# Kernel optimization log

Hardware: AMD Instinct MI355X
Metric: run time of the kernel (lower is better)

## Reference

```python
import jax, jax.numpy as jnp
import numpy as np

EPS = 1e-5


def setup_inputs() -> dict:
    key = jax.random.key(0)
    k_x, k_y, k_w, k_b = jax.random.split(key, 4)
    B, IN, OUT = 16384, 1024, 1024
    x = jax.random.normal(k_x, (B, IN), dtype=jnp.float32)
    y = jax.random.normal(k_y, (B, OUT), dtype=jnp.float32)
    # nn.Linear default init scale ~ 1/sqrt(in_features); keep activations sane
    weight = jax.random.normal(k_w, (OUT, IN), dtype=jnp.float32) / np.sqrt(IN)
    bias = jax.random.normal(k_b, (OUT,), dtype=jnp.float32) / np.sqrt(IN)
    gamma = jnp.ones((OUT,), dtype=jnp.float32)
    beta = jnp.zeros((OUT,), dtype=jnp.float32)
    return {"x": x, "y": y, "weight": weight, "bias": bias, "gamma": gamma, "beta": beta}


def reference(x, y, weight, bias, gamma, beta):
    # Linear: z[b, o] = sum_i x[b, i] * weight[o, i] + bias[o]
    z = jnp.einsum('bi,oi->bo', x, weight) + bias
    # LayerNorm over the feature (out_features) dim, biased variance
    mean = jnp.mean(z, axis=-1, keepdims=True)
    var = jnp.mean(jnp.square(z), axis=-1, keepdims=True) - jnp.square(mean)
    ln = (z - mean) * jax.lax.rsqrt(var + EPS) * gamma + beta
    # residual add then elementwise multiply
    return (ln + y) * y
```

## Files before the change

### kernel.cpp

```cpp
#include <hip/hip_runtime.h>
#include <stdint.h>

typedef unsigned short u16;
typedef __attribute__((ext_vector_type(8))) short short8;
typedef __attribute__((ext_vector_type(4))) float floatx4;
typedef __attribute__((ext_vector_type(2))) float floatx2;

#define K_DIM 1024
#define N_DIM 1024
#define BM 64
#define BK 32
#define NCHUNK (K_DIM / BK)

__device__ __forceinline__ u16 f2b(float f) {
    union { float f; uint32_t i; } v; v.f = f;
    uint32_t u = v.i;
    return (u16)((u + 0x7FFFu + ((u >> 16) & 1u)) >> 16);
}
__device__ __forceinline__ float b2f(u16 u) {
    union { uint32_t i; float f; } v; v.i = ((uint32_t)u) << 16; return v.f;
}

__global__ __launch_bounds__(256) void pack_w_kernel(const float* __restrict__ w,
                                                     u16* __restrict__ wpk) {
    int gid  = blockIdx.x * 256 + threadIdx.x;
    int lane = gid & 63;
    int kc   = (gid >> 6) & 31;
    int tile = gid >> 11;
    int n = tile * 16 + (lane & 15);
    int k = kc * 32 + (lane >> 4) * 8;
    const float* src = w + (size_t)n * K_DIM + k;
    floatx4 a = *(const floatx4*)(src);
    floatx4 b = *(const floatx4*)(src + 4);
    short8 o;
    o[0] = (short)f2b(a[0]); o[1] = (short)f2b(a[1]);
    o[2] = (short)f2b(a[2]); o[3] = (short)f2b(a[3]);
    o[4] = (short)f2b(b[0]); o[5] = (short)f2b(b[1]);
    o[6] = (short)f2b(b[2]); o[7] = (short)f2b(b[3]);
    *(short8*)(wpk + (size_t)gid * 8) = o;
}

__global__ __launch_bounds__(1024) void fused_gemm_ln_kernel(
    const float* __restrict__ x, const float* __restrict__ y,
    const u16* __restrict__ wpk, const float* __restrict__ bias,
    const float* __restrict__ gamma, const float* __restrict__ beta,
    float* __restrict__ out)
{
    __shared__ __align__(16) u16 lds_a[2][BM * BK];
    __shared__ __align__(16) u16 zbuf[16 * 1024];
    __shared__ float ls_sum[64];
    __shared__ float ls_sum2[64];
    __shared__ float ls_mean[64];
    __shared__ float ls_rs[64];

    const int tid  = threadIdx.x;
    const int lane = tid & 63;
    const int wv   = tid >> 6;
    const int q    = lane >> 4;
    const int row0 = blockIdx.x * BM;

    if (tid < 64) { ls_sum[tid] = 0.0f; ls_sum2[tid] = 0.0f; }

    const int sr = tid >> 4;
    const int sk = (tid & 15) << 1;
    const float* s_src = x + (size_t)(row0 + sr) * K_DIM + sk;
    const int s_qs  = (sk >> 3) ^ ((sr >> 1) & 3);
    const int s_off = sr * 64 + s_qs * 16 + (sk & 7) * 2;

    const u16* bp = wpk + (size_t)wv * 65536 + lane * 8;

    const int a_base = (lane & 15) * 64 + (q ^ (((lane & 15) >> 1) & 3)) * 16;

    floatx4 acc[4][4];
#pragma unroll
    for (int mi = 0; mi < 4; ++mi)
#pragma unroll
        for (int ni = 0; ni < 4; ++ni)
            acc[mi][ni] = (floatx4){0.0f, 0.0f, 0.0f, 0.0f};

    {
        floatx2 v0 = *(const floatx2*)(s_src);
        uint32_t p = (uint32_t)f2b(v0[0]) | ((uint32_t)f2b(v0[1]) << 16);
        *(uint32_t*)((char*)(&lds_a[0][0]) + s_off) = p;
    }
    floatx2 va_next = *(const floatx2*)(s_src + BK);
    floatx2 va_far  = *(const floatx2*)(s_src + 2 * BK);

    short8 bfr[2][4];
#pragma unroll
    for (int ni = 0; ni < 4; ++ni)
        bfr[0][ni] = *(const short8*)(bp + ni * 16384);

    __syncthreads();

#pragma unroll 2
    for (int kc = 0; kc < NCHUNK; ++kc) {
        const int cur = kc & 1;
        const int nxt = cur ^ 1;
        const char* ab = (const char*)(&lds_a[cur][0]);
        const int kn = (kc + 1 < NCHUNK) ? (kc + 1) : kc;

        short8 af0 = *(const short8*)(ab + a_base);
        short8 af1 = *(const short8*)(ab + a_base + 1024);
        bfr[nxt][0] = *(const short8*)(bp + 0 * 16384 + kn * 512);
        bfr[nxt][1] = *(const short8*)(bp + 1 * 16384 + kn * 512);
        const int ka = (kc + 3 < NCHUNK) ? (kc + 3) : (NCHUNK - 1);
        floatx2 vnew = *(const floatx2*)(s_src + ka * BK);

        __builtin_amdgcn_s_barrier();
        asm volatile("s_waitcnt lgkmcnt(0)" ::: "memory");
        __builtin_amdgcn_s_setprio(1);
#pragma unroll
        for (int ni = 0; ni < 4; ++ni) {
            acc[0][ni] = __builtin_amdgcn_mfma_f32_16x16x32_bf16(
                af0, bfr[cur][ni], acc[0][ni], 0, 0, 0);
            acc[1][ni] = __builtin_amdgcn_mfma_f32_16x16x32_bf16(
                af1, bfr[cur][ni], acc[1][ni], 0, 0, 0);
        }
        __builtin_amdgcn_s_setprio(0);
        __builtin_amdgcn_s_barrier();

        short8 af2 = *(const short8*)(ab + a_base + 2048);
        short8 af3 = *(const short8*)(ab + a_base + 3072);
        bfr[nxt][2] = *(const short8*)(bp + 2 * 16384 + kn * 512);
        bfr[nxt][3] = *(const short8*)(bp + 3 * 16384 + kn * 512);
        {
            uint32_t p = (uint32_t)f2b(va_next[0]) | ((uint32_t)f2b(va_next[1]) << 16);
            *(uint32_t*)((char*)(&lds_a[nxt][0]) + s_off) = p;
            va_next = va_far;
            va_far  = vnew;
        }

        __builtin_amdgcn_s_barrier();
        asm volatile("s_waitcnt lgkmcnt(0)" ::: "memory");
        __builtin_amdgcn_s_setprio(1);
#pragma unroll
        for (int ni = 0; ni < 4; ++ni) {
            acc[2][ni] = __builtin_amdgcn_mfma_f32_16x16x32_bf16(
                af2, bfr[cur][ni], acc[2][ni], 0, 0, 0);
            acc[3][ni] = __builtin_amdgcn_mfma_f32_16x16x32_bf16(
                af3, bfr[cur][ni], acc[3][ni], 0, 0, 0);
        }
        __builtin_amdgcn_s_setprio(0);
        __builtin_amdgcn_s_barrier();
    }

    float bias_v[4];
#pragma unroll
    for (int ni = 0; ni < 4; ++ni)
        bias_v[ni] = bias[(wv << 6) + (ni << 4) + (lane & 15)];
#pragma unroll
    for (int mi = 0; mi < 4; ++mi)
#pragma unroll
        for (int ni = 0; ni < 4; ++ni)
#pragma unroll
            for (int r = 0; r < 4; ++r)
                acc[mi][ni][r] += bias_v[ni];

#pragma unroll
    for (int mi = 0; mi < 4; ++mi)
#pragma unroll
        for (int r = 0; r < 4; ++r) {
            float s = 0.0f, s2 = 0.0f;
#pragma unroll
            for (int ni = 0; ni < 4; ++ni) {
                float v = acc[mi][ni][r];
                s += v; s2 += v * v;
            }
#pragma unroll
            for (int m = 1; m < 16; m <<= 1) {
                s  += __shfl_xor(s,  m, 64);
                s2 += __shfl_xor(s2, m, 64);
            }
            if ((lane & 15) == 0) {
                int rl = (mi << 4) + (q << 2) + r;
                atomicAdd(&ls_sum[rl], s);
                atomicAdd(&ls_sum2[rl], s2);
            }
        }

    __syncthreads();
    if (tid < 64) {
        float mean = ls_sum[tid] * (1.0f / 1024.0f);
        float var  = ls_sum2[tid] * (1.0f / 1024.0f) - mean * mean;
        ls_mean[tid] = mean;
        ls_rs[tid]   = rsqrtf(var + 1e-5f);
    }

    for (int mi = 0; mi < 4; ++mi) {
#pragma unroll
        for (int ni = 0; ni < 4; ++ni)
#pragma unroll
            for (int r = 0; r < 4; ++r) {
                int lr   = (q << 2) + r;
                int lin  = (((wv << 6) + (ni << 4) + (lane & 15)) << 1);
                int phys = lr * 2048 + (lin ^ (q << 5));
                *(u16*)((char*)zbuf + phys) = f2b(acc[mi][ni][r]);
            }
        __syncthreads();
#pragma unroll
        for (int it = 0; it < 2; ++it) {
            int row  = (tid >> 7) + (it << 3);
            int c8   = tid & 127;
            int phys = row * 2048 + ((c8 << 4) ^ (((row >> 2) & 3) << 5));
            short8 z8 = *(const short8*)((const char*)zbuf + phys);
            int grow  = row0 + (mi << 4) + row;
            float mean = ls_mean[(mi << 4) + row];
            float rs   = ls_rs[(mi << 4) + row];
            const float* yp = y     + (size_t)grow * N_DIM + c8 * 8;
            const float* gp = gamma + c8 * 8;
            const float* bpv = beta + c8 * 8;
            float*       op = out   + (size_t)grow * N_DIM + c8 * 8;
            floatx4 y0 = *(const floatx4*)(yp);
            floatx4 y1 = *(const floatx4*)(yp + 4);
            floatx4 g0 = *(const floatx4*)(gp);
            floatx4 g1 = *(const floatx4*)(gp + 4);
            floatx4 b0 = *(const floatx4*)(bpv);
            floatx4 b1 = *(const floatx4*)(bpv + 4);
            floatx4 o0, o1;
#pragma unroll
            for (int e = 0; e < 4; ++e) {
                float zv = b2f((u16)z8[e]);
                o0[e] = ((zv - mean) * rs * g0[e] + b0[e] + y0[e]) * y0[e];
            }
#pragma unroll
            for (int e = 0; e < 4; ++e) {
                float zv = b2f((u16)z8[e + 4]);
                o1[e] = ((zv - mean) * rs * g1[e] + b1[e] + y1[e]) * y1[e];
            }
            *(floatx4*)(op)     = o0;
            *(floatx4*)(op + 4) = o1;
        }
        __syncthreads();
    }
}

extern "C" void kernel_launch(void* const* d_in, const int* in_sizes, int n_in,
                              void* d_out, int out_size, void* d_ws, size_t ws_size,
                              hipStream_t stream) {
    const float* x     = (const float*)d_in[0];
    const float* y     = (const float*)d_in[1];
    const float* wgt   = (const float*)d_in[2];
    const float* bias  = (const float*)d_in[3];
    const float* gamma = (const float*)d_in[4];
    const float* beta  = (const float*)d_in[5];
    float* out = (float*)d_out;
    u16* wpk = (u16*)d_ws;

    pack_w_kernel<<<512, 256, 0, stream>>>(wgt, wpk);

    const int M = in_sizes[0] / K_DIM;
    fused_gemm_ln_kernel<<<M / BM, 1024, 0, stream>>>(x, y, wpk, bias, gamma, beta, out);
}
```

Before: 217.9 us.

## Stage half of the A operand in LDS and drop per-chunk barriers

Replaces the double-buffered per-chunk A staging, which used four block barriers per K chunk, with a bulk load of half the K dimension (16 chunks) into a larger LDS buffer. The main loop then runs without barriers, and there are only two syncs at the halfway point plus one before the epilogue. This removes per-iteration synchronisation overhead across the 16 waves, but the x loads are no longer overlapped with MFMA work and LDS use rises by 64KB, which may reduce occupancy.

New measurement: 216.9 us. About the same (-0.4%).

```diff
diff --git a/kernel.cpp b/kernel.cpp
--- a/kernel.cpp
+++ b/kernel.cpp
@@ -11,6 +11,7 @@
 #define BM 64
 #define BK 32
 #define NCHUNK (K_DIM / BK)
+#define HCHUNK (NCHUNK / 2)
 
 __device__ __forceinline__ u16 f2b(float f) {
     union { float f; uint32_t i; } v; v.f = f;
@@ -46,7 +47,7 @@
     const float* __restrict__ gamma, const float* __restrict__ beta,
     float* __restrict__ out)
 {
-    __shared__ __align__(16) u16 lds_a[2][BM * BK];
+    __shared__ __align__(16) u16 lds16[HCHUNK * BM * BK];
     __shared__ __align__(16) u16 zbuf[16 * 1024];
     __shared__ float ls_sum[64];
     __shared__ float ls_sum2[64];
@@ -78,13 +79,12 @@
         for (int ni = 0; ni < 4; ++ni)
             acc[mi][ni] = (floatx4){0.0f, 0.0f, 0.0f, 0.0f};
 
-    {
-        floatx2 v0 = *(const floatx2*)(s_src);
-        uint32_t p = (uint32_t)f2b(v0[0]) | ((uint32_t)f2b(v0[1]) << 16);
-        *(uint32_t*)((char*)(&lds_a[0][0]) + s_off) = p;
-    }
-    floatx2 va_next = *(const floatx2*)(s_src + BK);
-    floatx2 va_far  = *(const floatx2*)(s_src + 2 * BK);
+#pragma unroll 4
+    for (int c = 0; c < HCHUNK; ++c) {
+        floatx2 v = *(const floatx2*)(s_src + c * BK);
+        uint32_t p = (uint32_t)f2b(v[0]) | ((uint32_t)f2b(v[1]) << 16);
+        *(uint32_t*)((char*)lds16 + c * 4096 + s_off) = p;
+    }
 
     short8 bfr[2][4];
 #pragma unroll
@@ -93,56 +93,47 @@
 
     __syncthreads();
 
+    for (int half = 0; half < 2; ++half) {
+        if (half == 1) {
+            __syncthreads();
+#pragma unroll 4
+            for (int c = 0; c < HCHUNK; ++c) {
+                floatx2 v = *(const floatx2*)(s_src + (HCHUNK + c) * BK);
+                uint32_t p = (uint32_t)f2b(v[0]) | ((uint32_t)f2b(v[1]) << 16);
+                *(uint32_t*)((char*)lds16 + c * 4096 + s_off) = p;
+            }
+            __syncthreads();
+        }
+
 #pragma unroll 2
-    for (int kc = 0; kc < NCHUNK; ++kc) {
-        const int cur = kc & 1;
-        const int nxt = cur ^ 1;
-        const char* ab = (const char*)(&lds_a[cur][0]);
-        const int kn = (kc + 1 < NCHUNK) ? (kc + 1) : kc;
-
-        short8 af0 = *(const short8*)(ab + a_base);
-        short8 af1 = *(const short8*)(ab + a_base + 1024);
-        bfr[nxt][0] = *(const short8*)(bp + 0 * 16384 + kn * 512);
-        bfr[nxt][1] = *(const short8*)(bp + 1 * 16384 + kn * 512);
-        const int ka = (kc + 3 < NCHUNK) ? (kc + 3) : (NCHUNK - 1);
-        floatx2 vnew = *(const floatx2*)(s_src + ka * BK);
-
-        __builtin_amdgcn_s_barrier();
-        asm volatile("s_waitcnt lgkmcnt(0)" ::: "memory");
-        __builtin_amdgcn_s_setprio(1);
-#pragma unroll
-        for (int ni = 0; ni < 4; ++ni) {
-            acc[0][ni] = __builtin_amdgcn_mfma_f32_16x16x32_bf16(
-                af0, bfr[cur][ni], acc[0][ni], 0, 0, 0);
-            acc[1][ni] = __builtin_amdgcn_mfma_f32_16x16x32_bf16(
-                af1, bfr[cur][ni], acc[1][ni], 0, 0, 0);
-        }
-        __builtin_amdgcn_s_setprio(0);
-        __builtin_amdgcn_s_barrier();
-
-        short8 af2 = *(const short8*)(ab + a_base + 2048);
-        short8 af3 = *(const short8*)(ab + a_base + 3072);
-        bfr[nxt][2] = *(const short8*)(bp + 2 * 16384 + kn * 512);
-        bfr[nxt][3] = *(const short8*)(bp + 3 * 16384 + kn * 512);
-        {
-            uint32_t p = (uint32_t)f2b(va_next[0]) | ((uint32_t)f2b(va_next[1]) << 16);
-            *(uint32_t*)((char*)(&lds_a[nxt][0]) + s_off) = p;
-            va_next = va_far;
-            va_far  = vnew;
-        }
-
-        __builtin_amdgcn_s_barrier();
-        asm volatile("s_waitcnt lgkmcnt(0)" ::: "memory");
-        __builtin_amdgcn_s_setprio(1);
-#pragma unroll
-        for (int ni = 0; ni < 4; ++ni) {
-            acc[2][ni] = __builtin_amdgcn_mfma_f32_16x16x32_bf16(
-                af2, bfr[cur][ni], acc[2][ni], 0, 0, 0);
-            acc[3][ni] = __builtin_amdgcn_mfma_f32_16x16x32_bf16(
-                af3, bfr[cur][ni], acc[3][ni], 0, 0, 0);
-        }
-        __builtin_amdgcn_s_setprio(0);
-        __builtin_amdgcn_s_barrier();
+        for (int c = 0; c < HCHUNK; ++c) {
+            const int kc  = half * HCHUNK + c;
+            const int cur = kc & 1;
+            const int nxt = cur ^ 1;
+            const char* ab = (const char*)lds16 + c * 4096;
+
+            short8 af0 = *(const short8*)(ab + a_base);
+            short8 af1 = *(const short8*)(ab + a_base + 1024);
+            short8 af2 = *(const short8*)(ab + a_base + 2048);
+            short8 af3 = *(const short8*)(ab + a_base + 3072);
+
+            const int kn = (kc + 1 < NCHUNK) ? (kc + 1) : kc;
+#pragma unroll
+            for (int ni = 0; ni < 4; ++ni)
+                bfr[nxt][ni] = *(const short8*)(bp + ni * 16384 + kn * 512);
+
+#pragma unroll
+            for (int ni = 0; ni < 4; ++ni) {
+                acc[0][ni] = __builtin_amdgcn_mfma_f32_16x16x32_bf16(
+                    af0, bfr[cur][ni], acc[0][ni], 0, 0, 0);
+                acc[1][ni] = __builtin_amdgcn_mfma_f32_16x16x32_bf16(
+                    af1, bfr[cur][ni], acc[1][ni], 0, 0, 0);
+                acc[2][ni] = __builtin_amdgcn_mfma_f32_16x16x32_bf16(
+                    af2, bfr[cur][ni], acc[2][ni], 0, 0, 0);
+                acc[3][ni] = __builtin_amdgcn_mfma_f32_16x16x32_bf16(
+                    af3, bfr[cur][ni], acc[3][ni], 0, 0, 0);
+            }
+        }
     }
 
     float bias_v[4];
@@ -156,6 +147,8 @@
 #pragma unroll
             for (int r = 0; r < 4; ++r)
                 acc[mi][ni][r] += bias_v[ni];
+
+    __syncthreads();
 
 #pragma unroll
     for (int mi = 0; mi < 4; ++mi)
```
